# Optimization experiments

Measured on AMD Instinct MI355X. Metric: run time of the kernel, lower is better.

The kernel has to match this reference:

```python
import jax, jax.numpy as jnp
import numpy as np

MIN_NORM = 1e-15
PROJ_EPS = 4e-3


def _artanh(x):
    x = jnp.clip(x, -1 + 1e-7, 1 - 1e-7)
    return 0.5 * (jnp.log1p(x) - jnp.log1p(-x))


def _norm(x):
    return jnp.clip(jnp.linalg.norm(x, axis=-1, keepdims=True), MIN_NORM)


def proj(x, c):
    norm = _norm(x)
    maxnorm = (1.0 - PROJ_EPS) / jnp.sqrt(c)
    return jnp.where(norm > maxnorm, x / norm * maxnorm, x)


def expmap0(u, c):
    sqrt_c = jnp.sqrt(c)
    u_norm = _norm(u)
    return jnp.tanh(sqrt_c * u_norm) * u / (sqrt_c * u_norm)


def logmap0(p, c):
    sqrt_c = jnp.sqrt(c)
    p_norm = _norm(p)
    return _artanh(sqrt_c * p_norm) * p / (sqrt_c * p_norm)


def mobius_add(x, y, c):
    x2 = jnp.sum(x * x, axis=-1, keepdims=True)
    y2 = jnp.sum(y * y, axis=-1, keepdims=True)
    xy = jnp.sum(x * y, axis=-1, keepdims=True)
    num = (1 + 2 * c * xy + c * y2) * x + (1 - c * x2) * y
    denom = 1 + 2 * c * xy + c * c * x2 * y2
    return num / jnp.clip(denom, MIN_NORM)


def mobius_matvec(m, x, c):
    sqrt_c = jnp.sqrt(c)
    x_norm = _norm(x)
    mx = x @ m.T
    mx_norm = _norm(mx)
    res = jnp.tanh(mx_norm / x_norm * _artanh(sqrt_c * x_norm)) * mx / (mx_norm * sqrt_c)
    zero_row = jnp.all(mx == 0, axis=-1, keepdims=True)
    return jnp.where(zero_row, jnp.zeros_like(res), res)


def setup_inputs() -> dict:
    key = jax.random.key(0)
    k1, k2, k3, k4, k5 = jax.random.split(key, 5)
    n, d, e = 50000, 128, 800000
    c = jnp.float32(1.0)
    x = 0.1 * jax.random.normal(k1, (n, d), dtype=jnp.float32)
    x = proj(x, c)  # points on the Poincare ball
    adj = jax.random.randint(k2, (2, e), 0, n, dtype=jnp.int64)
    w = jax.random.uniform(k3, (e,), dtype=jnp.float32)
    weight = jax.random.normal(k4, (d, d), dtype=jnp.float32) * (1.0 / np.sqrt(d))
    bias = jax.random.normal(k5, (d,), dtype=jnp.float32) * 0.01
    return {"x": x, "adj": adj, "w": w, "weight": weight, "bias": bias}


def reference(x, adj, w, weight, bias):
    c_in = jnp.float32(1.0)
    c_out = jnp.float32(1.0)
    n = x.shape[0]

    # HypLinear (dropout p=0 -> identity on weight)
    mv = mobius_matvec(weight, x, c_in)
    res = proj(mv, c_in)
    b = bias.reshape(1, -1)  # proj_tan0 is identity on the Poincare ball
    hyp_bias = proj(expmap0(b, c_in), c_in)
    h = proj(mobius_add(res, hyp_bias, c_in), c_in)

    # HypAgg: logmap0 -> weighted segment_sum over edges -> expmap0 -> proj
    s, r = adj[0], adj[1]
    ht = logmap0(h, c_in)
    x_s = ht[s] * w[:, None]  # [E, d]
    x_agg = jax.ops.segment_sum(x_s, r, num_segments=n)
    h = proj(expmap0(x_agg, c_in), c_in)

    # HypAct: act(logmap0) -> expmap0 -> proj
    xt = jax.nn.relu(logmap0(h, c_in))
    out = proj(expmap0(xt, c_out), c_out)
    return (out, adj)
```

## Files before the change

### kernel.cpp

```cpp
#include <hip/hip_runtime.h>
#include <math.h>

#define MAXN 0.996f
#define MINN 1e-15f
#define CAPQ 1536

typedef __bf16   bf16x8  __attribute__((ext_vector_type(8)));
typedef _Float16 halfx8  __attribute__((ext_vector_type(8)));
typedef _Float16 half2_t __attribute__((ext_vector_type(2)));
typedef float    floatx4 __attribute__((ext_vector_type(4)));

__device__ __forceinline__ float wsum(float v){
  v += __shfl_xor(v, 32);
  v += __shfl_xor(v, 16);
  v += __shfl_xor(v, 8);
  v += __shfl_xor(v, 4);
  v += __shfl_xor(v, 2);
  v += __shfl_xor(v, 1);
  return v;
}

__device__ __forceinline__ float artanh_(float v){
  v = fminf(fmaxf(v, -1.f + 1e-7f), 1.f - 1e-7f);
  return 0.5f * (log1pf(v) - log1pf(-v));
}

__global__ __launch_bounds__(256)
void fusedA_kernel(const float* __restrict__ x, const float* __restrict__ W,
                   const float* __restrict__ bias, _Float16* __restrict__ ht, int n,
                   const int* __restrict__ adj, const float* __restrict__ w,
                   float* __restrict__ adj_out, int* __restrict__ bucketSize,
                   int2* __restrict__ part, int E, int nA)
{
  __shared__ __align__(16) char smem[32768];
  const int tid = threadIdx.x;

  if(blockIdx.x < nA){
    int* hist = (int*)smem;
    int* cur  = (int*)(smem + 4096);

#pragma unroll
    for(int k = 0; k < 4; k++) hist[k*256 + tid] = 0;
    __syncthreads();

    const int e0 = blockIdx.x * 4096;
    int p0r[16], p1r[16];
#pragma unroll
    for(int k = 0; k < 16; k++){
      int e = e0 + k*256 + tid;
      if(e < E){
        int s = adj[e];
        int r = adj[e + E];
        float we = w[e];
        adj_out[e]     = (float)s;
        adj_out[e + E] = (float)r;
        int bin = r >> 6;
        p0r[k] = s | ((r & 63) << 16) | (bin << 22);
        p1r[k] = __float_as_int(we);
        atomicAdd(&hist[bin], 1);
      }
    }
    __syncthreads();
#pragma unroll
    for(int k = 0; k < 4; k++){
      int bin = k*256 + tid;
      int c = hist[bin];
      cur[bin] = c ? atomicAdd(&bucketSize[bin], c) : 0;
    }
    __syncthreads();
#pragma unroll
    for(int k = 0; k < 16; k++){
      int e = e0 + k*256 + tid;
      if(e < E){
        int bin = ((unsigned)p0r[k]) >> 22;
        int pos = atomicAdd(&cur[bin], 1);
        if(pos < CAPQ) part[(size_t)bin * CAPQ + pos] = make_int2(p0r[k], p1r[k]);
      }
    }
    return;
  }

  __bf16* Wh = (__bf16*)smem;

  for(int g = tid; g < 2048; g += 256){
    int nr = g >> 4, k16 = g & 15;
    const float* wp = W + nr * 128 + k16 * 8;
    float4 a = *(const float4*)wp;
    float4 b = *(const float4*)(wp + 4);
    bf16x8 h;
    h[0]=(__bf16)a.x; h[1]=(__bf16)a.y; h[2]=(__bf16)a.z; h[3]=(__bf16)a.w;
    h[4]=(__bf16)b.x; h[5]=(__bf16)b.y; h[6]=(__bf16)b.z; h[7]=(__bf16)b.w;
    *(bf16x8*)&Wh[nr * 128 + ((k16 ^ (nr & 15)) << 3)] = h;
  }

  const int lane = tid & 63;
  const int wid  = tid >> 6;
  const int q    = lane >> 4;
  const int n15  = lane & 15;

  float b0 = bias[lane], b1 = bias[lane + 64];
  float bn = fmaxf(sqrtf(wsum(b0*b0 + b1*b1)), MINN);
  float sb = tanhf(bn) / bn;
  float hb0 = sb*b0, hb1 = sb*b1;
  float hnn = fmaxf(sqrtf(wsum(hb0*hb0 + hb1*hb1)), MINN);
  if(hnn > MAXN){ float f = MAXN/hnn; hb0 *= f; hb1 *= f; }
  const float y2 = wsum(hb0*hb0 + hb1*hb1);
  float hbv[8];
#pragma unroll
  for(int t = 0; t < 4; t++) hbv[t]     = __shfl(hb0, t*16 + n15);
#pragma unroll
  for(int t = 0; t < 4; t++) hbv[t + 4] = __shfl(hb1, t*16 + n15);

  __syncthreads();

  const int M0 = (blockIdx.x - nA) * 64 + wid * 16;
  if(M0 >= n) return;

  floatx4 acc[8];
#pragma unroll
  for(int t = 0; t < 8; t++) acc[t] = (floatx4){0.f,0.f,0.f,0.f};

  float x2p = 0.f;
  int m = M0 + n15; if(m > n - 1) m = n - 1;
#pragma unroll
  for(int kk = 0; kk < 4; kk++){
    const float* xp = x + (size_t)m * 128 + kk * 32 + q * 8;
    float4 xa = *(const float4*)xp;
    float4 xb = *(const float4*)(xp + 4);
    x2p += xa.x*xa.x + xa.y*xa.y + xa.z*xa.z + xa.w*xa.w
         + xb.x*xb.x + xb.y*xb.y + xb.z*xb.z + xb.w*xb.w;
    bf16x8 a;
    a[0]=(__bf16)xa.x; a[1]=(__bf16)xa.y; a[2]=(__bf16)xa.z; a[3]=(__bf16)xa.w;
    a[4]=(__bf16)xb.x; a[5]=(__bf16)xb.y; a[6]=(__bf16)xb.z; a[7]=(__bf16)xb.w;
    int k16 = kk * 4 + q;
#pragma unroll
    for(int t = 0; t < 8; t++){
      bf16x8 b = *(bf16x8*)&Wh[(t*16 + n15) * 128 + ((k16 ^ n15) << 3)];
      acc[t] = __builtin_amdgcn_mfma_f32_16x16x32_bf16(a, b, acc[t], 0, 0, 0);
    }
  }
  x2p += __shfl_xor(x2p, 16);
  x2p += __shfl_xor(x2p, 32);

  float mp[4], dp[4];
#pragma unroll
  for(int i = 0; i < 4; i++){
    float mpi = 0.f, dpi = 0.f;
#pragma unroll
    for(int t = 0; t < 8; t++){ float v = acc[t][i]; mpi = fmaf(v, v, mpi); dpi = fmaf(v, hbv[t], dpi); }
    mpi += __shfl_xor(mpi, 1); mpi += __shfl_xor(mpi, 2); mpi += __shfl_xor(mpi, 4); mpi += __shfl_xor(mpi, 8);
    dpi += __shfl_xor(dpi, 1); dpi += __shfl_xor(dpi, 2); dpi += __shfl_xor(dpi, 4); dpi += __shfl_xor(dpi, 8);
    mp[i] = mpi; dp[i] = dpi;
  }

  const int li   = lane & 3;
  const int srcl = (((lane >> 2) << 4) | li) & 63;
  float selmp = li==0 ? mp[0] : li==1 ? mp[1] : li==2 ? mp[2] : mp[3];
  float seldp = li==0 ? dp[0] : li==1 ? dp[1] : li==2 ? dp[2] : dp[3];
  float tmp_mp = __shfl(selmp, srcl);
  float tmp_dp = __shfl(seldp, srcl);
  float mxn = fmaxf(sqrtf(tmp_mp), MINN);
  float xn  = fmaxf(sqrtf(x2p), MINN);
  float tt  = tanhf(mxn / xn * artanh_(xn));
  float s1  = tt / mxn;
  float rn  = fmaxf(tt, MINN);
  if(rn > MAXN) s1 *= MAXN / rn;
  float xy    = s1 * tmp_dp;
  float r2    = s1 * s1 * tmp_mp;
  float alpha = 1.f + 2.f*xy + y2;
  float beta  = 1.f - r2;
  float inv   = 1.f / fmaxf(1.f + 2.f*xy + r2*y2, MINN);
  float as1   = alpha * s1;

  float as1b[4], betab[4], invb[4];
#pragma unroll
  for(int i = 0; i < 4; i++){
    int sl = ((lane >> 4) << 2) | i;
    as1b[i]  = __shfl(as1, sl);
    betab[i] = __shfl(beta, sl);
    invb[i]  = __shfl(inv, sl);
  }

  float uv[4][8];
  float u2[4];
#pragma unroll
  for(int i = 0; i < 4; i++){
    float u2i = 0.f;
#pragma unroll
    for(int t = 0; t < 8; t++){
      float u = (as1b[i] * acc[t][i] + betab[i] * hbv[t]) * invb[i];
      uv[i][t] = u;
      u2i = fmaf(u, u, u2i);
    }
    u2i += __shfl_xor(u2i, 1); u2i += __shfl_xor(u2i, 2); u2i += __shfl_xor(u2i, 4); u2i += __shfl_xor(u2i, 8);
    u2[i] = u2i;
  }

  float selu = li==0 ? u2[0] : li==1 ? u2[1] : li==2 ? u2[2] : u2[3];
  float tu   = __shfl(selu, srcl);
  float un = fmaxf(sqrtf(tu), MINN);
  float sc = 1.f, hn = un;
  if(un > MAXN){ sc = MAXN/un; hn = MAXN; }
  float lt = artanh_(hn) / hn * sc;

#pragma unroll
  for(int i = 0; i < 4; i++){
    int grow = M0 + q * 4 + i;
    float lti = __shfl(lt, ((lane >> 4) << 2) | i);
    if(grow < n){
      halfx8 f;
#pragma unroll
      for(int t = 0; t < 8; t++) f[t] = (_Float16)(lti * uv[i][t]);
      *(halfx8*)(ht + (size_t)grow * 128 + n15 * 8) = f;
    }
  }
}

__global__ __launch_bounds__(1024)
void aggB_kernel(const int* __restrict__ bucketSize, const int2* __restrict__ part,
                 const _Float16* __restrict__ ht, float* __restrict__ out, int n)
{
  __shared__ unsigned epk_l[CAPQ];
  __shared__ int hist[64];
  __shared__ int rowoff[65];
  __shared__ int cursor[64];
  __shared__ float tr[16][4][132];

  const int tid = threadIdx.x;
  const int b   = blockIdx.x;

  if(tid < 64) hist[tid] = 0;
  __syncthreads();

  int size = bucketSize[b]; if(size > CAPQ) size = CAPQ;
  const int2* src = part + (size_t)b * CAPQ;
  int2 e0v, e1v;
  const bool v0 = tid < size;
  const bool v1 = tid + 1024 < size;
  if(v0) e0v = src[tid];
  if(v1) e1v = src[tid + 1024];
  if(v0) atomicAdd(&hist[(((unsigned)e0v.x) >> 16) & 63], 1);
  if(v1) atomicAdd(&hist[(((unsigned)e1v.x) >> 16) & 63], 1);
  __syncthreads();
  if(tid < 64){
    int v = hist[tid];
    int iv = v;
#pragma unroll
    for(int o = 1; o < 64; o <<= 1){ int t = __shfl_up(iv, o); if(tid >= o) iv += t; }
    rowoff[tid + 1] = iv;
    cursor[tid]     = iv - v;
    if(tid == 0) rowoff[0] = 0;
  }
  __syncthreads();
#define PUTE(ev) { \
    int rl = (((unsigned)ev.x) >> 16) & 63; \
    int p = atomicAdd(&cursor[rl], 1); \
    unsigned wh = (unsigned)__builtin_bit_cast(unsigned short, \
                    (_Float16)__builtin_bit_cast(float, ev.y)); \
    epk_l[p] = (unsigned)(ev.x & 0xFFFF) | (wh << 16); }
  if(v0) PUTE(e0v);
  if(v1) PUTE(e1v);
#undef PUTE
  __syncthreads();

  const int gi   = tid >> 4;
  const int i    = tid & 15;
  const int wid  = tid >> 6;
  const int g    = (tid >> 4) & 3;
  const int row  = b * 64 + gi;
  const char* htb = (const char*)ht;
  const int ioff = i << 4;

  half2_t acc2[4];
#pragma unroll
  for(int k = 0; k < 4; k++) acc2[k] = (half2_t){(_Float16)0.f, (_Float16)0.f};

#define EDGE(pk) { \
    int s_ = (int)((pk) & 0xFFFFu); \
    half2_t w2_ = __builtin_bit_cast(half2_t, __builtin_amdgcn_perm(pk, pk, 0x03020302u)); \
    int4 q_ = *(const int4*)(htb + ((s_ << 8) | ioff)); \
    acc2[0] = __builtin_bit_cast(half2_t, q_.x) * w2_ + acc2[0]; \
    acc2[1] = __builtin_bit_cast(half2_t, q_.y) * w2_ + acc2[1]; \
    acc2[2] = __builtin_bit_cast(half2_t, q_.z) * w2_ + acc2[2]; \
    acc2[3] = __builtin_bit_cast(half2_t, q_.w) * w2_ + acc2[3]; \
  }

  if(row < n){
    int beg = rowoff[gi];
    int m   = rowoff[gi + 1] - beg;
    const unsigned* ep = epk_l + beg;
    int t = 0;
    for(; t + 3 < m; t += 4){
      unsigned pk0 = ep[t], pk1 = ep[t+1], pk2 = ep[t+2], pk3 = ep[t+3];
      EDGE(pk0); EDGE(pk1); EDGE(pk2); EDGE(pk3);
    }
    for(; t + 1 < m; t += 2){
      unsigned pk0 = ep[t], pk1 = ep[t+1];
      EDGE(pk0); EDGE(pk1);
    }
    if(t < m){ unsigned pk0 = ep[t]; EDGE(pk0); }
  }
#undef EDGE

  float acc[8];
#pragma unroll
  for(int k = 0; k < 4; k++){
    acc[2*k]   = (float)acc2[k][0];
    acc[2*k+1] = (float)acc2[k][1];
  }
  float u2p = 0.f;
#pragma unroll
  for(int k = 0; k < 8; k++) u2p = fmaf(acc[k], acc[k], u2p);
  u2p += __shfl_xor(u2p, 1); u2p += __shfl_xor(u2p, 2);
  u2p += __shfl_xor(u2p, 4); u2p += __shfl_xor(u2p, 8);
  float un = fmaxf(sqrtf(u2p), MINN);
  float te = tanhf(un);
  float se = te / un;
  float gn = fmaxf(te, MINN);
  float hn = gn;
  if(gn > MAXN){ se *= MAXN/gn; hn = MAXN; }
  float la = artanh_(hn) / hn * se;
  float l[8];
  float r2p = 0.f;
#pragma unroll
  for(int k = 0; k < 8; k++){ l[k] = fmaxf(la*acc[k], 0.f); r2p = fmaf(l[k], l[k], r2p); }
  r2p += __shfl_xor(r2p, 1); r2p += __shfl_xor(r2p, 2);
  r2p += __shfl_xor(r2p, 4); r2p += __shfl_xor(r2p, 8);
  float rn = fmaxf(sqrtf(r2p), MINN);
  float t2 = tanhf(rn);
  float s2 = t2 / rn;
  float on = fmaxf(t2, MINN);
  if(on > MAXN) s2 *= MAXN/on;

  if(row < n){
#pragma unroll
    for(int k = 0; k < 8; k++) tr[wid][g][k*16 + i] = s2 * l[k];
    float4 o0 = *(float4*)&tr[wid][g][i*8];
    float4 o1 = *(float4*)&tr[wid][g][i*8 + 4];
    float* orow = out + (size_t)row * 128 + i*8;
    *(float4*)orow       = o0;
    *(float4*)(orow + 4) = o1;
  }
}

extern "C" void kernel_launch(void* const* d_in, const int* in_sizes, int n_in,
                              void* d_out, int out_size, void* d_ws, size_t ws_size,
                              hipStream_t stream)
{
  const float* x    = (const float*)d_in[0];
  const int*   adj  = (const int*)  d_in[1];
  const float* w    = (const float*)d_in[2];
  const float* W    = (const float*)d_in[3];
  const float* bias = (const float*)d_in[4];
  const int n = in_sizes[0] / 128;
  const int E = in_sizes[2];

  float* out     = (float*)d_out;
  float* adj_out = out + (size_t)n * 128;

  char* ws = (char*)d_ws;
  _Float16* ht   = (_Float16*)ws;  ws += (size_t)n * 128 * sizeof(_Float16);
  int2*  part    = (int2*)ws;      ws += (size_t)1024 * CAPQ * sizeof(int2);
  int*   bucketSize = (int*)ws;

  const int nA = (E + 4095) / 4096;
  const int nS = (n + 63) / 64;
  const int nB = (n + 63) / 64;

  hipMemsetAsync(bucketSize, 0, 1024 * sizeof(int), stream);
  fusedA_kernel<<<nA + nS, 256, 0, stream>>>(x, W, bias, ht, n,
                                             adj, w, adj_out, bucketSize, part, E, nA);
  aggB_kernel<<<nB, 1024, 0, stream>>>(bucketSize, part, ht, out, n);
}
```

Before: 134.3 us.

## Stage ht stores through swizzled LDS and halve aggregation threads per row

In the fused A kernel, the per-lane half-precision ht stores are staged into a swizzled shared-memory tile, then written out as contiguous 16-byte row chunks, so global writes are coalesced. The early return is removed so every wave reaches the new barrier. The aggregation kernel now uses 512 threads with 8 lanes per row, each gathering 32 bytes per edge, and writes output directly without the LDS transpose. This trades more registers per thread and fewer threads in flight for wider per-lane gathers and less shared-memory traffic.

```diff
diff --git a/kernel.cpp b/kernel.cpp
--- a/kernel.cpp
+++ b/kernel.cpp
@@ -114,14 +114,13 @@
   __syncthreads();
 
   const int M0 = (blockIdx.x - nA) * 64 + wid * 16;
-  if(M0 >= n) return;
 
   floatx4 acc[8];
 #pragma unroll
   for(int t = 0; t < 8; t++) acc[t] = (floatx4){0.f,0.f,0.f,0.f};
 
   float x2p = 0.f;
-  int m = M0 + n15; if(m > n - 1) m = n - 1;
+  int m = M0 + n15; if(m > n - 1) m = n - 1; if(m < 0) m = 0;
 #pragma unroll
   for(int kk = 0; kk < 4; kk++){
     const float* xp = x + (size_t)m * 128 + kk * 32 + q * 8;
@@ -203,20 +202,31 @@
   if(un > MAXN){ sc = MAXN/un; hn = MAXN; }
   float lt = artanh_(hn) / hn * sc;
 
+  __syncthreads();
+  _Float16* scr = (_Float16*)(smem + (wid << 12));
+
 #pragma unroll
   for(int i = 0; i < 4; i++){
-    int grow = M0 + q * 4 + i;
+    int rl = q * 4 + i;
     float lti = __shfl(lt, ((lane >> 4) << 2) | i);
-    if(grow < n){
-      halfx8 f;
-#pragma unroll
-      for(int t = 0; t < 8; t++) f[t] = (_Float16)(lti * uv[i][t]);
-      *(halfx8*)(ht + (size_t)grow * 128 + n15 * 8) = f;
-    }
-  }
-}
-
-__global__ __launch_bounds__(1024)
+    int swz = (rl & 7) << 3;
+#pragma unroll
+    for(int t = 0; t < 8; t++){
+      scr[rl * 128 + ((t*16 + n15) ^ swz)] = (_Float16)(lti * uv[i][t]);
+    }
+  }
+#pragma unroll
+  for(int rep = 0; rep < 4; rep++){
+    int fb    = rep * 1024 + lane * 16;
+    int row   = fb >> 8;
+    int inner = fb & 255;
+    int grow2 = M0 + row;
+    halfx8 v = *(halfx8*)((char*)scr + row * 256 + (inner ^ ((row & 7) << 4)));
+    if(grow2 < n) *(halfx8*)((char*)ht + (size_t)grow2 * 256 + inner) = v;
+  }
+}
+
+__global__ __launch_bounds__(512)
 void aggB_kernel(const int* __restrict__ bucketSize, const int2* __restrict__ part,
                  const _Float16* __restrict__ ht, float* __restrict__ out, int n)
 {
@@ -224,7 +234,6 @@
   __shared__ int hist[64];
   __shared__ int rowoff[65];
   __shared__ int cursor[64];
-  __shared__ float tr[16][4][132];
 
   const int tid = threadIdx.x;
   const int b   = blockIdx.x;
@@ -234,13 +243,16 @@
 
   int size = bucketSize[b]; if(size > CAPQ) size = CAPQ;
   const int2* src = part + (size_t)b * CAPQ;
-  int2 e0v, e1v;
+  int2 e0v, e1v, e2v;
   const bool v0 = tid < size;
-  const bool v1 = tid + 1024 < size;
+  const bool v1 = tid + 512 < size;
+  const bool v2 = tid + 1024 < size;
   if(v0) e0v = src[tid];
-  if(v1) e1v = src[tid + 1024];
+  if(v1) e1v = src[tid + 512];
+  if(v2) e2v = src[tid + 1024];
   if(v0) atomicAdd(&hist[(((unsigned)e0v.x) >> 16) & 63], 1);
   if(v1) atomicAdd(&hist[(((unsigned)e1v.x) >> 16) & 63], 1);
+  if(v2) atomicAdd(&hist[(((unsigned)e2v.x) >> 16) & 63], 1);
   __syncthreads();
   if(tid < 64){
     int v = hist[tid];
@@ -260,29 +272,34 @@
     epk_l[p] = (unsigned)(ev.x & 0xFFFF) | (wh << 16); }
   if(v0) PUTE(e0v);
   if(v1) PUTE(e1v);
+  if(v2) PUTE(e2v);
 #undef PUTE
   __syncthreads();
 
-  const int gi   = tid >> 4;
-  const int i    = tid & 15;
-  const int wid  = tid >> 6;
-  const int g    = (tid >> 4) & 3;
+  const int gi   = tid >> 3;
+  const int i    = tid & 7;
   const int row  = b * 64 + gi;
   const char* htb = (const char*)ht;
-  const int ioff = i << 4;
-
-  half2_t acc2[4];
-#pragma unroll
-  for(int k = 0; k < 4; k++) acc2[k] = (half2_t){(_Float16)0.f, (_Float16)0.f};
+  const int ioff = i << 5;
+
+  half2_t acc2[8];
+#pragma unroll
+  for(int k = 0; k < 8; k++) acc2[k] = (half2_t){(_Float16)0.f, (_Float16)0.f};
 
 #define EDGE(pk) { \
     int s_ = (int)((pk) & 0xFFFFu); \
     half2_t w2_ = __builtin_bit_cast(half2_t, __builtin_amdgcn_perm(pk, pk, 0x03020302u)); \
-    int4 q_ = *(const int4*)(htb + ((s_ << 8) | ioff)); \
-    acc2[0] = __builtin_bit_cast(half2_t, q_.x) * w2_ + acc2[0]; \
-    acc2[1] = __builtin_bit_cast(half2_t, q_.y) * w2_ + acc2[1]; \
-    acc2[2] = __builtin_bit_cast(half2_t, q_.z) * w2_ + acc2[2]; \
-    acc2[3] = __builtin_bit_cast(half2_t, q_.w) * w2_ + acc2[3]; \
+    const char* p_ = htb + ((s_ << 8) | ioff); \
+    int4 qa = *(const int4*)p_; \
+    int4 qb = *(const int4*)(p_ + 16); \
+    acc2[0] = __builtin_bit_cast(half2_t, qa.x) * w2_ + acc2[0]; \
+    acc2[1] = __builtin_bit_cast(half2_t, qa.y) * w2_ + acc2[1]; \
+    acc2[2] = __builtin_bit_cast(half2_t, qa.z) * w2_ + acc2[2]; \
+    acc2[3] = __builtin_bit_cast(half2_t, qa.w) * w2_ + acc2[3]; \
+    acc2[4] = __builtin_bit_cast(half2_t, qb.x) * w2_ + acc2[4]; \
+    acc2[5] = __builtin_bit_cast(half2_t, qb.y) * w2_ + acc2[5]; \
+    acc2[6] = __builtin_bit_cast(half2_t, qb.z) * w2_ + acc2[6]; \
+    acc2[7] = __builtin_bit_cast(half2_t, qb.w) * w2_ + acc2[7]; \
   }
 
   if(row < n){
@@ -302,17 +319,16 @@
   }
 #undef EDGE
 
-  float acc[8];
-#pragma unroll
-  for(int k = 0; k < 4; k++){
+  float acc[16];
+#pragma unroll
+  for(int k = 0; k < 8; k++){
     acc[2*k]   = (float)acc2[k][0];
     acc[2*k+1] = (float)acc2[k][1];
   }
   float u2p = 0.f;
 #pragma unroll
-  for(int k = 0; k < 8; k++) u2p = fmaf(acc[k], acc[k], u2p);
-  u2p += __shfl_xor(u2p, 1); u2p += __shfl_xor(u2p, 2);
-  u2p += __shfl_xor(u2p, 4); u2p += __shfl_xor(u2p, 8);
+  for(int k = 0; k < 16; k++) u2p = fmaf(acc[k], acc[k], u2p);
+  u2p += __shfl_xor(u2p, 1); u2p += __shfl_xor(u2p, 2); u2p += __shfl_xor(u2p, 4);
   float un = fmaxf(sqrtf(u2p), MINN);
   float te = tanhf(un);
   float se = te / un;
@@ -320,12 +336,11 @@
   float hn = gn;
   if(gn > MAXN){ se *= MAXN/gn; hn = MAXN; }
   float la = artanh_(hn) / hn * se;
-  float l[8];
+  float l[16];
   float r2p = 0.f;
 #pragma unroll
-  for(int k = 0; k < 8; k++){ l[k] = fmaxf(la*acc[k], 0.f); r2p = fmaf(l[k], l[k], r2p); }
-  r2p += __shfl_xor(r2p, 1); r2p += __shfl_xor(r2p, 2);
-  r2p += __shfl_xor(r2p, 4); r2p += __shfl_xor(r2p, 8);
+  for(int k = 0; k < 16; k++){ l[k] = fmaxf(la*acc[k], 0.f); r2p = fmaf(l[k], l[k], r2p); }
+  r2p += __shfl_xor(r2p, 1); r2p += __shfl_xor(r2p, 2); r2p += __shfl_xor(r2p, 4);
   float rn = fmaxf(sqrtf(r2p), MINN);
   float t2 = tanhf(rn);
   float s2 = t2 / rn;
@@ -333,13 +348,14 @@
   if(on > MAXN) s2 *= MAXN/on;
 
   if(row < n){
-#pragma unroll
-    for(int k = 0; k < 8; k++) tr[wid][g][k*16 + i] = s2 * l[k];
-    float4 o0 = *(float4*)&tr[wid][g][i*8];
-    float4 o1 = *(float4*)&tr[wid][g][i*8 + 4];
-    float* orow = out + (size_t)row * 128 + i*8;
-    *(float4*)orow       = o0;
-    *(float4*)(orow + 4) = o1;
+    float* orow = out + (size_t)row * 128 + i * 16;
+#pragma unroll
+    for(int k = 0; k < 4; k++){
+      float4 o;
+      o.x = s2 * l[4*k];   o.y = s2 * l[4*k+1];
+      o.z = s2 * l[4*k+2]; o.w = s2 * l[4*k+3];
+      *(float4*)(orow + 4*k) = o;
+    }
   }
 }
 
@@ -370,5 +386,5 @@
   hipMemsetAsync(bucketSize, 0, 1024 * sizeof(int), stream);
   fusedA_kernel<<<nA + nS, 256, 0, stream>>>(x, W, bias, ht, n,
                                              adj, w, adj_out, bucketSize, part, E, nA);
-  aggB_kernel<<<nB, 1024, 0, stream>>>(bucketSize, part, ht, out, n);
-}
+  aggB_kernel<<<nB, 512, 0, stream>>>(bucketSize, part, ht, out, n);
+}
```

After: 134.2 us. About the same (-0.1%).
